# Kernel optimization log

Hardware: AMD Instinct MI355X
Metric: run time of the kernel (lower is better)

## Reference

```python
import jax, jax.numpy as jnp
import numpy as np

N = 50000      # nodes
E = 300000     # edges
F_IN = 128     # num_features
H = 256        # hidden_dim
C = 32         # num_classes


def gcn_conv(x, src, dst, W, b, num_nodes):
    """PyG-style GCNConv: add self-loops, sym-normalize, X W, scatter-add, + bias."""
    loop = jnp.arange(num_nodes, dtype=src.dtype)
    src2 = jnp.concatenate([src, loop])          # [E+N]
    dst2 = jnp.concatenate([dst, loop])          # [E+N]
    # degree of target nodes (with self-loops, unit edge weights)
    deg = jax.ops.segment_sum(jnp.ones_like(dst2, dtype=x.dtype), dst2,
                              num_segments=num_nodes)
    dinv = jnp.where(deg > 0, jax.lax.rsqrt(deg), 0.0)
    norm = dinv[src2] * dinv[dst2]               # [E+N]
    h = x @ W                                    # [N, out]  dense GEMM first (PyG order)
    msg = h[src2] * norm[:, None]                # gather + scale  [E+N, out]
    out = jax.ops.segment_sum(msg, dst2, num_segments=num_nodes)  # scatter-add
    return out + b


def setup_inputs() -> dict:
    key = jax.random.key(0)
    ks = jax.random.split(key, 8)
    x = jax.random.normal(ks[0], (N, F_IN), dtype=jnp.float32)
    edge_index = jax.random.randint(ks[1], (2, E), 0, N, dtype=jnp.int64)
    W1 = jax.random.normal(ks[2], (F_IN, H), dtype=jnp.float32) / np.float32(np.sqrt(F_IN))
    b1 = jnp.zeros((H,), jnp.float32)
    W2 = jax.random.normal(ks[3], (H, H), dtype=jnp.float32) / np.float32(np.sqrt(H))
    b2 = jnp.zeros((H,), jnp.float32)
    Wc = jax.random.normal(ks[4], (H, C), dtype=jnp.float32) / np.float32(np.sqrt(H))
    bc = jnp.zeros((C,), jnp.float32)
    return {"x": x, "edge_index": edge_index, "W1": W1, "b1": b1,
            "W2": W2, "b2": b2, "Wc": Wc, "bc": bc}


def reference(x, edge_index, W1, b1, W2, b2, Wc, bc):
    src, dst = edge_index[0], edge_index[1]
    h = gcn_conv(x, src, dst, W1, b1, N)
    h = jax.nn.relu(h)                 # dropout is identity in eval mode
    h = gcn_conv(h, src, dst, W2, b2, N)
    h = jax.nn.relu(h)
    return h @ Wc + bc                 # [N, C]
```

## Files before the change

kernel.cpp:

```cpp
#include <hip/hip_runtime.h>
#include <math.h>

using short8 = __attribute__((ext_vector_type(8))) short;
using f32x4 = __attribute__((ext_vector_type(4))) float;

#define CAP 48

__device__ inline short f2bf(float f) {
    unsigned u = __builtin_bit_cast(unsigned, f);
    unsigned r = (u + 0x7fffu + ((u >> 16) & 1u)) >> 16;
    return (short)r;
}
__device__ inline float bf2f(short s) {
    unsigned u = ((unsigned)(unsigned short)s) << 16;
    return __builtin_bit_cast(float, u);
}

typedef const void __attribute__((address_space(1))) gvoid_t;
typedef void __attribute__((address_space(3))) svoid_t;
__device__ inline void gload16(const short* g, short* l) {
    __builtin_amdgcn_global_load_lds((gvoid_t*)g, (svoid_t*)l, 16, 0, 0);
}


__global__ void prep_kernel(const float* __restrict__ x, const float* __restrict__ W1,
                            const float* __restrict__ W2, const float* __restrict__ Wc,
                            const int* __restrict__ src, const int* __restrict__ dst,
                            short* __restrict__ xb, short* __restrict__ Wt1,
                            short* __restrict__ Wt2, short* __restrict__ Wtc,
                            int* __restrict__ deg, int* __restrict__ eslot,
                            int n, int e) {
    int idx = blockIdx.x * blockDim.x + threadIdx.x;
    const int nx8 = n * 16;
    if (idx < nx8) {
        const float4* p = (const float4*)x + (size_t)idx * 2;
        float4 v0 = p[0], v1 = p[1];
        short8 o;
        o[0] = f2bf(v0.x); o[1] = f2bf(v0.y); o[2] = f2bf(v0.z); o[3] = f2bf(v0.w);
        o[4] = f2bf(v1.x); o[5] = f2bf(v1.y); o[6] = f2bf(v1.z); o[7] = f2bf(v1.w);
        ((short8*)xb)[idx] = o;
        return;
    }
    idx -= nx8;
    if (idx < 128 * 256) {
        int k = idx >> 8, c = idx & 255;
        Wt1[c * 128 + k] = f2bf(W1[idx]);
        return;
    }
    idx -= 128 * 256;
    if (idx < 256 * 256) {
        int k = idx >> 8, c = idx & 255;
        Wt2[c * 256 + k] = f2bf(W2[idx]);
        return;
    }
    idx -= 256 * 256;
    if (idx < 256 * 32) {
        int k = idx >> 5, c = idx & 31;
        Wtc[c * 256 + k] = f2bf(Wc[idx]);
        return;
    }
    idx -= 256 * 32;
    if (idx < e) {
        int d = dst[idx], s = src[idx];
        int pos = atomicAdd(&deg[d], 1);
        if (pos < CAP) eslot[(size_t)d * CAP + pos] = s;
    }
}


template<bool RELU_BF16OUT>
__global__ __launch_bounds__(256) void mfma_gemm128_kernel(
    const short* __restrict__ A, const short* __restrict__ Wt,
    const float* __restrict__ bias, void* __restrict__ Cout,
    int M, int K, int NC)
{
    __shared__ short As[128 * 32];
    __shared__ short Bs[128 * 32];

    const int tid = threadIdx.x;
    const int wave = tid >> 6, lane = tid & 63;
    const int m0 = blockIdx.y * 128, n0 = blockIdx.x * 128;
    const int wm = (wave >> 1) * 64, wn = (wave & 1) * 64;

    const int lr0 = tid >> 2;
    const int lr1 = 64 + lr0;
    const int cdst = tid & 3;
    const int cg0 = cdst ^ ((lr0 >> 1) & 3);
    const int cg1 = cdst ^ ((lr1 >> 1) & 3);
    int ga0 = m0 + lr0; if (ga0 >= M) ga0 = M - 1;
    int ga1 = m0 + lr1; if (ga1 >= M) ga1 = M - 1;
    int gb0 = n0 + lr0; if (gb0 >= NC) gb0 = NC - 1;
    int gb1 = n0 + lr1; if (gb1 >= NC) gb1 = NC - 1;
    const short* pa0 = A + (size_t)ga0 * K + cg0 * 8;
    const short* pa1 = A + (size_t)ga1 * K + cg1 * 8;
    const short* pb0 = Wt + (size_t)gb0 * K + cg0 * 8;
    const short* pb1 = Wt + (size_t)gb1 * K + cg1 * 8;

    short* lA0 = &As[(wave * 16) * 32];
    short* lA1 = &As[(64 + wave * 16) * 32];
    short* lB0 = &Bs[(wave * 16) * 32];
    short* lB1 = &Bs[(64 + wave * 16) * 32];

    f32x4 acc[4][4] = {};
    const int fr = lane & 15;
    const int cfrag = lane >> 4;
    const int swzr = (fr >> 1) & 3;

    for (int k0 = 0; k0 < K; k0 += 32) {
        gload16(pa0 + k0, lA0);
        gload16(pa1 + k0, lA1);
        gload16(pb0 + k0, lB0);
        gload16(pb1 + k0, lB1);
        __syncthreads();

        short8 af[4], bfv[4];
        #pragma unroll
        for (int mt = 0; mt < 4; ++mt) {
            int rr = wm + mt * 16 + fr;
            af[mt] = *(const short8*)&As[rr * 32 + ((cfrag ^ swzr) << 3)];
        }
        #pragma unroll
        for (int nt = 0; nt < 4; ++nt) {
            int rr = wn + nt * 16 + fr;
            bfv[nt] = *(const short8*)&Bs[rr * 32 + ((cfrag ^ swzr) << 3)];
        }

        #pragma unroll
        for (int mt = 0; mt < 4; ++mt)
            #pragma unroll
            for (int nt = 0; nt < 4; ++nt)
                acc[mt][nt] = __builtin_amdgcn_mfma_f32_16x16x32_bf16(
                    af[mt], bfv[nt], acc[mt][nt], 0, 0, 0);

        __syncthreads();
    }

    #pragma unroll
    for (int mt = 0; mt < 4; ++mt) {
        #pragma unroll
        for (int nt = 0; nt < 4; ++nt) {
            #pragma unroll
            for (int r = 0; r < 4; ++r) {
                int grow = m0 + wm + mt * 16 + (lane >> 4) * 4 + r;
                int gcol = n0 + wn + nt * 16 + (lane & 15);
                if (grow < M && gcol < NC) {
                    float v = acc[mt][nt][r] + bias[gcol];
                    if (RELU_BF16OUT)
                        ((short*)Cout)[(size_t)grow * NC + gcol] = f2bf(fmaxf(v, 0.f));
                    else
                        ((float*)Cout)[(size_t)grow * NC + gcol] = v;
                }
            }
        }
    }
}


__global__ __launch_bounds__(512) void gemm2c_kernel(
    const short* __restrict__ A,
    const short* __restrict__ Wt2,
    const float* __restrict__ b2,
    const short* __restrict__ Wtc,
    const float* __restrict__ bc,
    float* __restrict__ out,
    int M)
{
    const int K = 256;
    const int TP = 264;
    __shared__ short smem[128 * 264];
    short* As = smem;
    short* Bs = smem + 128 * 32;

    const int tid = threadIdx.x;
    const int wave = tid >> 6, lane = tid & 63;
    const int m0 = blockIdx.x * 128;
    const int wm = (wave >> 2) * 64;
    const int wn = (wave & 3) * 64;

    const int srow = lane >> 2;
    const int cdst = lane & 3;
    const int lrA  = wave * 16 + srow;
    const int lrB1 = 128 + lrA;
    int gaA = m0 + lrA; if (gaA >= M) gaA = M - 1;
    const int cgA  = cdst ^ ((lrA  >> 1) & 3);
    const int cgB1 = cdst ^ ((lrB1 >> 1) & 3);
    const short* pa  = A   + (size_t)gaA  * K + cgA  * 8;
    const short* pb0 = Wt2 + (size_t)lrA  * K + cgA  * 8;
    const short* pb1 = Wt2 + (size_t)lrB1 * K + cgB1 * 8;
    short* lA  = &As[(wave * 16) * 32];
    short* lB0 = &Bs[(wave * 16) * 32];
    short* lB1 = &Bs[(128 + wave * 16) * 32];

    f32x4 acc[4][4] = {};
    const int fr = lane & 15;
    const int cfrag = lane >> 4;
    const int swzr = (fr >> 1) & 3;

    for (int k0 = 0; k0 < K; k0 += 32) {
        gload16(pa  + k0, lA);
        gload16(pb0 + k0, lB0);
        gload16(pb1 + k0, lB1);
        __syncthreads();

        short8 af[4], bfv[4];
        #pragma unroll
        for (int mt = 0; mt < 4; ++mt) {
            int rr = wm + mt * 16 + fr;
            af[mt] = *(const short8*)&As[rr * 32 + ((cfrag ^ swzr) << 3)];
        }
        #pragma unroll
        for (int nt = 0; nt < 4; ++nt) {
            int rr = wn + nt * 16 + fr;
            bfv[nt] = *(const short8*)&Bs[rr * 32 + ((cfrag ^ swzr) << 3)];
        }

        #pragma unroll
        for (int mt = 0; mt < 4; ++mt)
            #pragma unroll
            for (int nt = 0; nt < 4; ++nt)
                acc[mt][nt] = __builtin_amdgcn_mfma_f32_16x16x32_bf16(
                    af[mt], bfv[nt], acc[mt][nt], 0, 0, 0);

        __syncthreads();
    }

    #pragma unroll
    for (int mt = 0; mt < 4; ++mt) {
        #pragma unroll
        for (int nt = 0; nt < 4; ++nt) {
            #pragma unroll
            for (int r = 0; r < 4; ++r) {
                int lrow = wm + mt * 16 + (lane >> 4) * 4 + r;
                int gcol = wn + nt * 16 + fr;
                float v = acc[mt][nt][r] + b2[gcol];
                smem[lrow * TP + gcol] = f2bf(fmaxf(v, 0.f));
            }
        }
    }
    __syncthreads();

    f32x4 c2[2] = {};
    const int fk = (lane >> 4) * 8;
    for (int k0 = 0; k0 < K; k0 += 32) {
        short8 a8 = *(const short8*)&smem[(wave * 16 + fr) * TP + fk + k0];
        #pragma unroll
        for (int nt = 0; nt < 2; ++nt) {
            short8 b8 = *(const short8*)(Wtc + (size_t)(nt * 16 + fr) * K + fk + k0);
            c2[nt] = __builtin_amdgcn_mfma_f32_16x16x32_bf16(a8, b8, c2[nt], 0, 0, 0);
        }
    }
    #pragma unroll
    for (int nt = 0; nt < 2; ++nt) {
        #pragma unroll
        for (int r = 0; r < 4; ++r) {
            int grow = m0 + wave * 16 + (lane >> 4) * 4 + r;
            int gcol = nt * 16 + fr;
            if (grow < M)
                out[(size_t)grow * 32 + gcol] = c2[nt][r] + bc[gcol];
        }
    }
}


template<int LPN>
__global__ __launch_bounds__(256) void gather_kernel(
    const short* __restrict__ h, const int* __restrict__ deg,
    const int* __restrict__ eslot, short* __restrict__ out, int n)
{
    const int F = LPN * 8;
    int node = (blockIdx.x * 256 + threadIdx.x) / LPN;
    if (node >= n) return;
    int lane = threadIdx.x % LPN;
    int f = lane * 8;

    int dg = deg[node];
    if (dg > CAP) dg = CAP;
    float di = rsqrtf((float)dg + 1.0f);
    float w = di * di;

    const size_t rb = (size_t)node * F + f;
    short8 hv = *(const short8*)(h + rb);
    float a[8];
    #pragma unroll
    for (int j = 0; j < 8; ++j) a[j] = bf2f(hv[j]) * w;

    const int* bucket = eslot + (size_t)node * CAP;
    for (int e = 0; e < dg; e += 4) {
        int4 s4 = *(const int4*)(bucket + e);
        int i0 = s4.x;
        int i1 = (e + 1 < dg) ? s4.y : 0;
        int i2 = (e + 2 < dg) ? s4.z : 0;
        int i3 = (e + 3 < dg) ? s4.w : 0;
        int d0 = deg[i0], d1 = deg[i1], d2 = deg[i2], d3 = deg[i3];
        short8 v0 = *(const short8*)(h + (size_t)i0 * F + f);
        short8 v1 = *(const short8*)(h + (size_t)i1 * F + f);
        short8 v2 = *(const short8*)(h + (size_t)i2 * F + f);
        short8 v3 = *(const short8*)(h + (size_t)i3 * F + f);
        float w0 = rsqrtf((float)d0 + 1.0f) * di;
        float w1 = (e + 1 < dg) ? rsqrtf((float)d1 + 1.0f) * di : 0.f;
        float w2 = (e + 2 < dg) ? rsqrtf((float)d2 + 1.0f) * di : 0.f;
        float w3 = (e + 3 < dg) ? rsqrtf((float)d3 + 1.0f) * di : 0.f;
        #pragma unroll
        for (int j = 0; j < 8; ++j) {
            a[j] = fmaf(bf2f(v0[j]), w0, a[j]);
            a[j] = fmaf(bf2f(v1[j]), w1, a[j]);
            a[j] = fmaf(bf2f(v2[j]), w2, a[j]);
            a[j] = fmaf(bf2f(v3[j]), w3, a[j]);
        }
    }
    short8 o;
    #pragma unroll
    for (int j = 0; j < 8; ++j) o[j] = f2bf(a[j]);
    *(short8*)(out + rb) = o;
}


extern "C" void kernel_launch(void* const* d_in, const int* in_sizes, int n_in,
                              void* d_out, int out_size, void* d_ws, size_t ws_size,
                              hipStream_t stream) {
    const float* x  = (const float*)d_in[0];
    const int*   ei = (const int*)d_in[1];
    const float* W1 = (const float*)d_in[2];
    const float* b1 = (const float*)d_in[3];
    const float* W2 = (const float*)d_in[4];
    const float* b2 = (const float*)d_in[5];
    const float* Wc = (const float*)d_in[6];
    const float* bc = (const float*)d_in[7];
    float* out = (float*)d_out;

    const int E = in_sizes[1] / 2;
    const int N = in_sizes[0] / 128;
    const int F_IN = 128, H = 256;
    const int* src = ei;
    const int* dst = ei + E;

    short* xb   = (short*)d_ws;
    short* aggX = xb + (size_t)N * 128;
    short* hA   = aggX + (size_t)N * 128;
    short* hB   = hA + (size_t)N * 256;
    short* Wt1  = hB + (size_t)N * 256;
    short* Wt2  = Wt1 + 256 * 128;
    short* Wtc  = Wt2 + 256 * 256;
    int*   deg  = (int*)(Wtc + 32 * 256);
    int*   eslot= deg + N;

    const int TB = 256;

    hipMemsetAsync(deg, 0, (size_t)N * sizeof(int), stream);

    const int prep_total = N * 16 + 128 * 256 + 256 * 256 + 256 * 32 + E;
    prep_kernel<<<(prep_total + TB - 1) / TB, TB, 0, stream>>>(
        x, W1, W2, Wc, src, dst, xb, Wt1, Wt2, Wtc, deg, eslot, N, E);

    const int gy = (N + 127) / 128;

    gather_kernel<16><<<((size_t)N * 16 + TB - 1) / TB, TB, 0, stream>>>(
        xb, deg, eslot, aggX, N);
    mfma_gemm128_kernel<true><<<dim3(H / 128, gy), 256, 0, stream>>>(aggX, Wt1, b1, hA, N, F_IN, H);

    gather_kernel<32><<<((size_t)N * 32 + TB - 1) / TB, TB, 0, stream>>>(
        hA, deg, eslot, hB, N);
    gemm2c_kernel<<<gy, 512, 0, stream>>>(hB, Wt2, b2, Wtc, bc, out, N);
}
```

Measured before the change: 203.5 us.

## Fuse layer-2 neighbor gather into the GEMM2+classifier kernel via LDS

The second-layer aggregation now runs inside the layer-2 GEMM kernel. Each block gathers and normalizes its 128 nodes' neighbor rows directly into a swizzled LDS tile, so the intermediate hB buffer no longer makes a round trip through HBM and one launch disappears. Wt2 tiles are also prefetched one k-step ahead with the sync moved. The costs are a much larger LDS footprint (about 80KB per block) and only 391 blocks of 512 threads doing the latency-bound gather, which may reduce occupancy and parallelism compared with the standalone gather kernel.

Result: faster. 195.1 us (-4.1%).

```diff
diff --git a/kernel.cpp b/kernel.cpp
--- a/kernel.cpp
+++ b/kernel.cpp
@@ -156,8 +156,9 @@
 }
 
 
-__global__ __launch_bounds__(512) void gemm2c_kernel(
-    const short* __restrict__ A,
+__global__ __launch_bounds__(512, 4) void layer2_fused_kernel(
+    const short* __restrict__ hA,
+    const int* __restrict__ deg, const int* __restrict__ eslot,
     const short* __restrict__ Wt2,
     const float* __restrict__ b2,
     const short* __restrict__ Wtc,
@@ -166,47 +167,91 @@
     int M)
 {
     const int K = 256;
-    const int TP = 264;
-    __shared__ short smem[128 * 264];
-    short* As = smem;
-    short* Bs = smem + 128 * 32;
+    __shared__ short smem[128 * 256 + 256 * 32];
+    short* hT = smem;
+    short* Bs = smem + 128 * 256;
 
     const int tid = threadIdx.x;
     const int wave = tid >> 6, lane = tid & 63;
     const int m0 = blockIdx.x * 128;
+
+    const int srow = tid >> 2;
+    const int cdst = tid & 3;
+    const int lrB0 = srow, lrB1 = 128 + srow;
+    const int cg0 = cdst ^ ((lrB0 >> 1) & 3);
+    const int cg1 = cdst ^ ((lrB1 >> 1) & 3);
+    const short* pb0 = Wt2 + (size_t)lrB0 * K + cg0 * 8;
+    const short* pb1 = Wt2 + (size_t)lrB1 * K + cg1 * 8;
+    short* lB0 = &Bs[(wave * 16) * 32];
+    short* lB1 = &Bs[(128 + wave * 16) * 32];
+
+    gload16(pb0, lB0);
+    gload16(pb1, lB1);
+
+    {
+        const int grp = tid >> 5;
+        const int gl  = tid & 31;
+        const int f   = gl * 8;
+        const int wslot = (gl >> 2) * 32;
+        for (int r0 = 0; r0 < 128; r0 += 16) {
+            int r = r0 + grp;
+            int node = m0 + r; if (node >= M) node = M - 1;
+            int dg = deg[node];
+            if (dg > CAP) dg = CAP;
+            float di = rsqrtf((float)dg + 1.0f);
+            float w = di * di;
+            short8 hv = *(const short8*)(hA + (size_t)node * 256 + f);
+            float a[8];
+            #pragma unroll
+            for (int j = 0; j < 8; ++j) a[j] = bf2f(hv[j]) * w;
+
+            const int* bucket = eslot + (size_t)node * CAP;
+            for (int e = 0; e < dg; e += 4) {
+                int4 s4 = *(const int4*)(bucket + e);
+                int i0 = s4.x;
+                int i1 = (e + 1 < dg) ? s4.y : 0;
+                int i2 = (e + 2 < dg) ? s4.z : 0;
+                int i3 = (e + 3 < dg) ? s4.w : 0;
+                int d0 = deg[i0], d1 = deg[i1], d2 = deg[i2], d3 = deg[i3];
+                short8 v0 = *(const short8*)(hA + (size_t)i0 * 256 + f);
+                short8 v1 = *(const short8*)(hA + (size_t)i1 * 256 + f);
+                short8 v2 = *(const short8*)(hA + (size_t)i2 * 256 + f);
+                short8 v3 = *(const short8*)(hA + (size_t)i3 * 256 + f);
+                float w0 = rsqrtf((float)d0 + 1.0f) * di;
+                float w1 = (e + 1 < dg) ? rsqrtf((float)d1 + 1.0f) * di : 0.f;
+                float w2 = (e + 2 < dg) ? rsqrtf((float)d2 + 1.0f) * di : 0.f;
+                float w3 = (e + 3 < dg) ? rsqrtf((float)d3 + 1.0f) * di : 0.f;
+                #pragma unroll
+                for (int j = 0; j < 8; ++j) {
+                    a[j] = fmaf(bf2f(v0[j]), w0, a[j]);
+                    a[j] = fmaf(bf2f(v1[j]), w1, a[j]);
+                    a[j] = fmaf(bf2f(v2[j]), w2, a[j]);
+                    a[j] = fmaf(bf2f(v3[j]), w3, a[j]);
+                }
+            }
+            short8 o;
+            #pragma unroll
+            for (int j = 0; j < 8; ++j) o[j] = f2bf(a[j]);
+            int slot = (gl & 3) ^ ((r >> 1) & 3);
+            *(short8*)&hT[r * 256 + wslot + slot * 8] = o;
+        }
+    }
+
     const int wm = (wave >> 2) * 64;
     const int wn = (wave & 3) * 64;
-
-    const int srow = lane >> 2;
-    const int cdst = lane & 3;
-    const int lrA  = wave * 16 + srow;
-    const int lrB1 = 128 + lrA;
-    int gaA = m0 + lrA; if (gaA >= M) gaA = M - 1;
-    const int cgA  = cdst ^ ((lrA  >> 1) & 3);
-    const int cgB1 = cdst ^ ((lrB1 >> 1) & 3);
-    const short* pa  = A   + (size_t)gaA  * K + cgA  * 8;
-    const short* pb0 = Wt2 + (size_t)lrA  * K + cgA  * 8;
-    const short* pb1 = Wt2 + (size_t)lrB1 * K + cgB1 * 8;
-    short* lA  = &As[(wave * 16) * 32];
-    short* lB0 = &Bs[(wave * 16) * 32];
-    short* lB1 = &Bs[(128 + wave * 16) * 32];
-
-    f32x4 acc[4][4] = {};
     const int fr = lane & 15;
     const int cfrag = lane >> 4;
     const int swzr = (fr >> 1) & 3;
 
+    f32x4 acc[4][4] = {};
     for (int k0 = 0; k0 < K; k0 += 32) {
-        gload16(pa  + k0, lA);
-        gload16(pb0 + k0, lB0);
-        gload16(pb1 + k0, lB1);
         __syncthreads();
 
         short8 af[4], bfv[4];
         #pragma unroll
         for (int mt = 0; mt < 4; ++mt) {
             int rr = wm + mt * 16 + fr;
-            af[mt] = *(const short8*)&As[rr * 32 + ((cfrag ^ swzr) << 3)];
+            af[mt] = *(const short8*)&hT[rr * 256 + k0 + ((cfrag ^ swzr) << 3)];
         }
         #pragma unroll
         for (int nt = 0; nt < 4; ++nt) {
@@ -214,14 +259,18 @@
             bfv[nt] = *(const short8*)&Bs[rr * 32 + ((cfrag ^ swzr) << 3)];
         }
 
+        __syncthreads();
+        if (k0 + 32 < K) {
+            gload16(pb0 + k0 + 32, lB0);
+            gload16(pb1 + k0 + 32, lB1);
+        }
+
         #pragma unroll
         for (int mt = 0; mt < 4; ++mt)
             #pragma unroll
             for (int nt = 0; nt < 4; ++nt)
                 acc[mt][nt] = __builtin_amdgcn_mfma_f32_16x16x32_bf16(
                     af[mt], bfv[nt], acc[mt][nt], 0, 0, 0);
-
-        __syncthreads();
     }
 
     #pragma unroll
@@ -233,19 +282,22 @@
                 int lrow = wm + mt * 16 + (lane >> 4) * 4 + r;
                 int gcol = wn + nt * 16 + fr;
                 float v = acc[mt][nt][r] + b2[gcol];
-                smem[lrow * TP + gcol] = f2bf(fmaxf(v, 0.f));
+                int slot = ((gcol >> 3) & 3) ^ ((lrow >> 1) & 3);
+                hT[lrow * 256 + (gcol >> 5) * 32 + slot * 8 + (gcol & 7)] =
+                    f2bf(fmaxf(v, 0.f));
             }
         }
     }
     __syncthreads();
 
     f32x4 c2[2] = {};
-    const int fk = (lane >> 4) * 8;
     for (int k0 = 0; k0 < K; k0 += 32) {
-        short8 a8 = *(const short8*)&smem[(wave * 16 + fr) * TP + fk + k0];
+        int row = wave * 16 + fr;
+        short8 a8 = *(const short8*)&hT[row * 256 + k0 + ((cfrag ^ swzr) << 3)];
         #pragma unroll
         for (int nt = 0; nt < 2; ++nt) {
-            short8 b8 = *(const short8*)(Wtc + (size_t)(nt * 16 + fr) * K + fk + k0);
+            short8 b8 = *(const short8*)(Wtc + (size_t)(nt * 16 + fr) * K +
+                                         (cfrag << 3) + k0);
             c2[nt] = __builtin_amdgcn_mfma_f32_16x16x32_bf16(a8, b8, c2[nt], 0, 0, 0);
         }
     }
@@ -337,8 +389,7 @@
     short* xb   = (short*)d_ws;
     short* aggX = xb + (size_t)N * 128;
     short* hA   = aggX + (size_t)N * 128;
-    short* hB   = hA + (size_t)N * 256;
-    short* Wt1  = hB + (size_t)N * 256;
+    short* Wt1  = hA + (size_t)N * 256;
     short* Wt2  = Wt1 + 256 * 128;
     short* Wtc  = Wt2 + 256 * 256;
     int*   deg  = (int*)(Wtc + 32 * 256);
@@ -358,7 +409,6 @@
         xb, deg, eslot, aggX, N);
     mfma_gemm128_kernel<true><<<dim3(H / 128, gy), 256, 0, stream>>>(aggX, Wt1, b1, hA, N, F_IN, H);
 
-    gather_kernel<32><<<((size_t)N * 32 + TB - 1) / TB, TB, 0, stream>>>(
-        hA, deg, eslot, hB, N);
-    gemm2c_kernel<<<gy, 512, 0, stream>>>(hB, Wt2, b2, Wtc, bc, out, N);
-}
+    layer2_fused_kernel<<<gy, 512, 0, stream>>>(
+        hA, deg, eslot, Wt2, b2, Wtc, bc, out, N);
+}
```
